# Performance work log

Hardware: AMD Instinct MI355X
Metric: run time of the kernel (lower is better)

## Reference

```python
import jax, jax.numpy as jnp
import numpy as np

H = 64  # hidden size

def _gru_layer(x_tbi, w_ih, w_hh, b_ih, b_hh):
    # x_tbi: [T,B,I]; w_ih: [3H,I]; w_hh: [3H,H]; biases: [3H]
    # Precompute all input projections in one big GEMM: [T,B,3H]
    gx_all = jnp.einsum('tbi,gi->tbg', x_tbi, w_ih) + b_ih

    def step(h, gx):
        gh = h @ w_hh.T + b_hh                      # [B,3H]
        xr, xz, xn = jnp.split(gx, 3, axis=-1)
        hr, hz, hn = jnp.split(gh, 3, axis=-1)
        r = jax.nn.sigmoid(xr + hr)
        z = jax.nn.sigmoid(xz + hz)
        n = jnp.tanh(xn + r * hn)
        h_new = (1.0 - z) * n + z * h
        return h_new, h_new

    B = x_tbi.shape[1]
    h0 = jnp.zeros((B, H), dtype=x_tbi.dtype)
    h_last, out = jax.lax.scan(step, h0, gx_all)     # out: [T,B,H]
    return out, h_last


def setup_inputs() -> dict:
    key = jax.random.key(0)
    ks = jax.random.split(key, 11)
    B, T, I = 2048, 1024, 1
    s0 = 1.0 / np.sqrt(H)  # PyTorch GRU init scale
    u = lambda k, shape: jax.random.uniform(k, shape, jnp.float32, -s0, s0)
    return {
        'x': jax.random.normal(ks[0], (B, T, I), jnp.float32),
        'w_ih0': u(ks[1], (3 * H, I)),
        'w_hh0': u(ks[2], (3 * H, H)),
        'b_ih0': u(ks[3], (3 * H,)),
        'b_hh0': u(ks[4], (3 * H,)),
        'w_ih1': u(ks[5], (3 * H, H)),
        'w_hh1': u(ks[6], (3 * H, H)),
        'b_ih1': u(ks[7], (3 * H,)),
        'b_hh1': u(ks[8], (3 * H,)),
        'w_fc': u(ks[9], (1, H)),
        'b_fc': u(ks[10], (1,)),
    }


def reference(x, w_ih0, w_hh0, b_ih0, b_hh0, w_ih1, w_hh1, b_ih1, b_hh1, w_fc, b_fc):
    # x: [B,T,1] (batch_first) -> scan over time axis
    x_tbi = jnp.transpose(x, (1, 0, 2))              # [T,B,1]
    out0, _ = _gru_layer(x_tbi, w_ih0, w_hh0, b_ih0, b_hh0)   # [T,B,H]
    _, h_last = _gru_layer(out0, w_ih1, w_hh1, b_ih1, b_hh1)  # [B,H]
    # fc(out[:, -1, :]) == fc(h_last of top layer)
    return h_last @ w_fc.T + b_fc                    # [B,1]
```

## Files before the change

kernel.cpp:

```cpp
#include <hip/hip_runtime.h>

#define H    64
#define TT   1024
#define MB   8
#define NW   512
#define NWG  256
#define GSP  584
#define HRUS 144

typedef float  f32x4  __attribute__((ext_vector_type(4)));
typedef __bf16 bf16x8 __attribute__((ext_vector_type(8)));

__device__ __forceinline__ unsigned short bf16_rne(float f) {
    unsigned u = __float_as_uint(f);
    u += 0x7FFFu + ((u >> 16) & 1u);
    return (unsigned short)(u >> 16);
}
__device__ __forceinline__ float fast_sigmoid(float x) {
    return __builtin_amdgcn_rcpf(1.0f + __expf(-x));
}
__device__ __forceinline__ float fast_tanh(float x) {
    float xx = fminf(fmaxf(x, -15.0f), 15.0f);
    float e  = __expf(2.0f * xx);
    return (e - 1.0f) * __builtin_amdgcn_rcpf(e + 1.0f);
}

__global__ __launch_bounds__(NW, 2) void gru_mfma3(
    const float* __restrict__ x,
    const float* __restrict__ w_ih0, const float* __restrict__ w_hh0,
    const float* __restrict__ b_ih0, const float* __restrict__ b_hh0,
    const float* __restrict__ w_ih1, const float* __restrict__ w_hh1,
    const float* __restrict__ b_ih1, const float* __restrict__ b_hh1,
    const float* __restrict__ w_fc,  const float* __restrict__ b_fc,
    float* __restrict__ out)
{
    __shared__ __align__(16) float          xs[MB * TT];
    __shared__ __align__(16) float          gA[MB * GSP];
    __shared__ __align__(16) unsigned short hA[16 * HRUS];

    const int tid  = threadIdx.x;
    const int wave = tid >> 6;
    const int lane = tid & 63;
    const int r    = lane & 15;
    const int q    = lane >> 4;
    const int b0g  = blockIdx.x * MB;

    for (int i = tid; i < 16*HRUS; i += NW) hA[i] = 0;
    for (int i = tid; i < MB*GSP;  i += NW) gA[i] = 0.0f;

    {
        const float* xrow = x + (size_t)(b0g + wave) * TT;
        float* xd = xs + wave * TT;
        #pragma unroll
        for (int u = 0; u < 4; ++u) {
            int idx = (u * 64 + lane) * 4;
            *(float4*)(xd + idx) = *(const float4*)(xrow + idx);
        }
    }

    bf16x8 whi[5][2], wlo[5][2];
    int   doff [5];
    bool  wr_ok[5];
    #pragma unroll
    for (int i = 0; i < 5; ++i) {
        const int n = 5 * wave + i;
        const float* W; int gr;
        if      (n < 12) { W = w_hh0; gr = 16 * n; }
        else if (n < 24) { W = w_ih1; gr = 16 * (n - 12); }
        else if (n < 36) { W = w_hh1; gr = 16 * (n - 24); }
        else             { W = w_hh0; gr = 0; }
        #pragma unroll
        for (int c = 0; c < 2; ++c) {
            const float* wp = W + (gr + r) * H + 32 * c + 8 * q;
            float4 p0 = *(const float4*)wp;
            float4 p1 = *(const float4*)(wp + 4);
            float f[8] = {p0.x,p0.y,p0.z,p0.w,p1.x,p1.y,p1.z,p1.w};
            unsigned short uh[8], ul[8];
            #pragma unroll
            for (int j = 0; j < 8; ++j) {
                unsigned short h16 = bf16_rne(f[j]);
                uh[j] = h16;
                ul[j] = bf16_rne(f[j] - __uint_as_float((unsigned)h16 << 16));
            }
            whi[i][c] = *(const bf16x8*)uh;
            wlo[i][c] = *(const bf16x8*)ul;
        }
        doff [i] = (r & 7) * GSP + 16 * n + 4 * q;
        wr_ok[i] = (n < 36) && ((n < 24) == (r < 8));
    }

    const unsigned short* hp0 = hA + r * HRUS + 8 * q;
    const unsigned short* hp1 = hA + r * HRUS + 8 * (4 + q);
    const unsigned short* hp2 = hp0 + 64;
    const unsigned short* hp3 = hp1 + 64;

    unsigned short* p0h = hA + wave * HRUS + lane;
    unsigned short* p0l = p0h + 64;
    unsigned short* p1h = hA + (wave + 8) * HRUS + lane;
    unsigned short* p1l = p1h + 64;

    const float* gp  = gA + wave * GSP;
    const float* xmy = xs + wave * TT;

    const float wi0r = w_ih0[lane], wi0z = w_ih0[64+lane], wi0n = w_ih0[128+lane];
    const float c0r  = b_ih0[lane]     + b_hh0[lane];
    const float c0z  = b_ih0[64+lane]  + b_hh0[64+lane];
    const float bi0n = b_ih0[128+lane], bh0n = b_hh0[128+lane];
    const float c1r  = b_ih1[lane]     + b_hh1[lane];
    const float c1z  = b_ih1[64+lane]  + b_hh1[64+lane];
    const float bi1n = b_ih1[128+lane], bh1n = b_hh1[128+lane];
    const float wfc  = w_fc[lane];

    float h0reg = 0.0f, h1reg = 0.0f;
    __syncthreads();

    #pragma unroll 1
    for (int t = 0; t < TT; ++t) {
        if (t > 0) {
            float xr = gp[192+lane], xz = gp[256+lane], xn = gp[320+lane];
            float hr = gp[384+lane], hz = gp[448+lane], hn = gp[512+lane];
            float rr = fast_sigmoid(xr + hr + c1r);
            float zz = fast_sigmoid(xz + hz + c1z);
            float nn = fast_tanh(xn + bi1n + rr * (hn + bh1n));
            h1reg = fmaf(zz, h1reg - nn, nn);
            unsigned short hh = bf16_rne(h1reg);
            *p1h = hh;
            *p1l = bf16_rne(h1reg - __uint_as_float((unsigned)hh << 16));
        }
        {
            float xv  = xmy[t];
            float g0r = gp[lane], g0z = gp[64+lane], g0n = gp[128+lane];
            float rr = fast_sigmoid(fmaf(xv, wi0r, c0r) + g0r);
            float zz = fast_sigmoid(fmaf(xv, wi0z, c0z) + g0z);
            float nn = fast_tanh(fmaf(xv, wi0n, bi0n) + rr * (g0n + bh0n));
            h0reg = fmaf(zz, h0reg - nn, nn);
            unsigned short hh = bf16_rne(h0reg);
            *p0h = hh;
            *p0l = bf16_rne(h0reg - __uint_as_float((unsigned)hh << 16));
        }
        __syncthreads();

        {
            bf16x8 hhi0 = *(const bf16x8*)hp0;
            bf16x8 hhi1 = *(const bf16x8*)hp1;
            bf16x8 hlo0 = *(const bf16x8*)hp2;
            bf16x8 hlo1 = *(const bf16x8*)hp3;
            #pragma unroll
            for (int i = 0; i < 5; ++i) {
                f32x4 d = {0.0f, 0.0f, 0.0f, 0.0f};
                d = __builtin_amdgcn_mfma_f32_16x16x32_bf16(whi[i][0], hhi0, d, 0,0,0);
                d = __builtin_amdgcn_mfma_f32_16x16x32_bf16(whi[i][1], hhi1, d, 0,0,0);
                d = __builtin_amdgcn_mfma_f32_16x16x32_bf16(whi[i][0], hlo0, d, 0,0,0);
                d = __builtin_amdgcn_mfma_f32_16x16x32_bf16(whi[i][1], hlo1, d, 0,0,0);
                d = __builtin_amdgcn_mfma_f32_16x16x32_bf16(wlo[i][0], hhi0, d, 0,0,0);
                d = __builtin_amdgcn_mfma_f32_16x16x32_bf16(wlo[i][1], hhi1, d, 0,0,0);
                if (wr_ok[i]) {
                    *(f32x4*)(gA + doff[i]) = d;
                }
            }
        }
        __syncthreads();
    }

    {
        float xr = gp[192+lane], xz = gp[256+lane], xn = gp[320+lane];
        float hr = gp[384+lane], hz = gp[448+lane], hn = gp[512+lane];
        float rr = fast_sigmoid(xr + hr + c1r);
        float zz = fast_sigmoid(xz + hz + c1z);
        float nn = fast_tanh(xn + bi1n + rr * (hn + bh1n));
        h1reg = fmaf(zz, h1reg - nn, nn);
    }
    {
        float v = h1reg * wfc;
        #pragma unroll
        for (int s = 32; s > 0; s >>= 1) v += __shfl_xor(v, s, 64);
        if (lane == 0) out[b0g + wave] = v + b_fc[0];
    }
}

extern "C" void kernel_launch(void* const* d_in, const int* in_sizes, int n_in,
                              void* d_out, int out_size, void* d_ws, size_t ws_size,
                              hipStream_t stream) {
    (void)in_sizes; (void)n_in; (void)out_size; (void)d_ws; (void)ws_size;
    gru_mfma3<<<NWG, NW, 0, stream>>>(
        (const float*)d_in[0],
        (const float*)d_in[1], (const float*)d_in[2],
        (const float*)d_in[3], (const float*)d_in[4],
        (const float*)d_in[5], (const float*)d_in[6],
        (const float*)d_in[7], (const float*)d_in[8],
        (const float*)d_in[9], (const float*)d_in[10],
        (float*)d_out);
}
```

Before: 976.4 us.

## Fuse gate nonlinearity into MFMA waves with double-buffered hidden state, one barrier per step

Waves are split into two groups. Four waves own layer 0 and four own layer 1, and each wave computes a 16-unit slice of all three gates with MFMA and applies the GRU nonlinearity directly from the accumulator registers. This removes the shared-memory gate scratch buffer and its round trip. The hidden state is double-buffered, so each timestep needs one barrier instead of two. The cost is that half of each MFMA tile (rows for batches 8-15) is wasted, and the layer-1 waves do twice the MFMA work of the layer-0 waves, so the load is unbalanced. The final output is reconstructed from the bf16 hi/lo pair instead of the fp32 register, which slightly changes precision.

```diff
diff --git a/kernel.cpp b/kernel.cpp
--- a/kernel.cpp
+++ b/kernel.cpp
@@ -2,10 +2,8 @@
 
 #define H    64
 #define TT   1024
-#define MB   8
 #define NW   512
 #define NWG  256
-#define GSP  584
 #define HRUS 144
 
 typedef float  f32x4  __attribute__((ext_vector_type(4)));
@@ -25,7 +23,7 @@
     return (e - 1.0f) * __builtin_amdgcn_rcpf(e + 1.0f);
 }
 
-__global__ __launch_bounds__(NW, 2) void gru_mfma3(
+__global__ __launch_bounds__(NW, 2) void gru_fuse6(
     const float* __restrict__ x,
     const float* __restrict__ w_ih0, const float* __restrict__ w_hh0,
     const float* __restrict__ b_ih0, const float* __restrict__ b_hh0,
@@ -34,20 +32,24 @@
     const float* __restrict__ w_fc,  const float* __restrict__ b_fc,
     float* __restrict__ out)
 {
-    __shared__ __align__(16) float          xs[MB * TT];
-    __shared__ __align__(16) float          gA[MB * GSP];
-    __shared__ __align__(16) unsigned short hA[16 * HRUS];
+    __shared__ __align__(16) float          xs[8 * TT];
+    __shared__ __align__(16) unsigned short hB[2][16 * HRUS];
 
     const int tid  = threadIdx.x;
     const int wave = tid >> 6;
     const int lane = tid & 63;
     const int r    = lane & 15;
     const int q    = lane >> 4;
-    const int b0g  = blockIdx.x * MB;
-
-    for (int i = tid; i < 16*HRUS; i += NW) hA[i] = 0;
-    for (int i = tid; i < MB*GSP;  i += NW) gA[i] = 0.0f;
-
+    const int b    = r & 7;
+    const int b0g  = blockIdx.x * 8;
+    const bool grpB = (wave >= 4);
+    const int  w4   = wave & 3;
+    const int  jb   = 16 * w4 + 4 * q;
+
+    {
+        unsigned short* hz = &hB[0][0];
+        for (int i = tid; i < 2 * 16 * HRUS; i += NW) hz[i] = 0;
+    }
     {
         const float* xrow = x + (size_t)(b0g + wave) * TT;
         float* xd = xs + wave * TT;
@@ -58,20 +60,14 @@
         }
     }
 
-    bf16x8 whi[5][2], wlo[5][2];
-    int   doff [5];
-    bool  wr_ok[5];
+    bf16x8 whi[6][2], wlo[6][2];
     #pragma unroll
-    for (int i = 0; i < 5; ++i) {
-        const int n = 5 * wave + i;
-        const float* W; int gr;
-        if      (n < 12) { W = w_hh0; gr = 16 * n; }
-        else if (n < 24) { W = w_ih1; gr = 16 * (n - 12); }
-        else if (n < 36) { W = w_hh1; gr = 16 * (n - 24); }
-        else             { W = w_hh0; gr = 0; }
+    for (int i = 0; i < 6; ++i) {
+        const float* W = grpB ? ((i < 3) ? w_ih1 : w_hh1) : w_hh0;
+        const int row0 = 64 * (i % 3) + 16 * w4;
         #pragma unroll
         for (int c = 0; c < 2; ++c) {
-            const float* wp = W + (gr + r) * H + 32 * c + 8 * q;
+            const float* wp = W + (row0 + r) * H + 32 * c + 8 * q;
             float4 p0 = *(const float4*)wp;
             float4 p1 = *(const float4*)(wp + 4);
             float f[8] = {p0.x,p0.y,p0.z,p0.w,p1.x,p1.y,p1.z,p1.w};
@@ -85,93 +81,131 @@
             whi[i][c] = *(const bf16x8*)uh;
             wlo[i][c] = *(const bf16x8*)ul;
         }
-        doff [i] = (r & 7) * GSP + 16 * n + 4 * q;
-        wr_ok[i] = (n < 36) && ((n < 24) == (r < 8));
-    }
-
-    const unsigned short* hp0 = hA + r * HRUS + 8 * q;
-    const unsigned short* hp1 = hA + r * HRUS + 8 * (4 + q);
-    const unsigned short* hp2 = hp0 + 64;
-    const unsigned short* hp3 = hp1 + 64;
-
-    unsigned short* p0h = hA + wave * HRUS + lane;
-    unsigned short* p0l = p0h + 64;
-    unsigned short* p1h = hA + (wave + 8) * HRUS + lane;
-    unsigned short* p1l = p1h + 64;
-
-    const float* gp  = gA + wave * GSP;
-    const float* xmy = xs + wave * TT;
-
-    const float wi0r = w_ih0[lane], wi0z = w_ih0[64+lane], wi0n = w_ih0[128+lane];
-    const float c0r  = b_ih0[lane]     + b_hh0[lane];
-    const float c0z  = b_ih0[64+lane]  + b_hh0[64+lane];
-    const float bi0n = b_ih0[128+lane], bh0n = b_hh0[128+lane];
-    const float c1r  = b_ih1[lane]     + b_hh1[lane];
-    const float c1z  = b_ih1[64+lane]  + b_hh1[64+lane];
-    const float bi1n = b_ih1[128+lane], bh1n = b_hh1[128+lane];
-    const float wfc  = w_fc[lane];
-
-    float h0reg = 0.0f, h1reg = 0.0f;
+    }
+
+    float gwr[4], gwz[4], gwn[4], gcr[4], gcz[4], gbn[4], ghn[4];
+    #pragma unroll
+    for (int k = 0; k < 4; ++k) {
+        const int j = jb + k;
+        if (grpB) {
+            gwr[k] = gwz[k] = gwn[k] = 0.0f;
+            gcr[k] = b_ih1[j]      + b_hh1[j];
+            gcz[k] = b_ih1[64+j]   + b_hh1[64+j];
+            gbn[k] = b_ih1[128+j];
+            ghn[k] = b_hh1[128+j];
+        } else {
+            gwr[k] = w_ih0[j]; gwz[k] = w_ih0[64+j]; gwn[k] = w_ih0[128+j];
+            gcr[k] = b_ih0[j]      + b_hh0[j];
+            gcz[k] = b_ih0[64+j]   + b_hh0[64+j];
+            gbn[k] = b_ih0[128+j];
+            ghn[k] = b_hh0[128+j];
+        }
+    }
+    const float wfc = w_fc[lane];
+
+    float hst[4] = {0.0f, 0.0f, 0.0f, 0.0f};
     __syncthreads();
 
     #pragma unroll 1
-    for (int t = 0; t < TT; ++t) {
-        if (t > 0) {
-            float xr = gp[192+lane], xz = gp[256+lane], xn = gp[320+lane];
-            float hr = gp[384+lane], hz = gp[448+lane], hn = gp[512+lane];
-            float rr = fast_sigmoid(xr + hr + c1r);
-            float zz = fast_sigmoid(xz + hz + c1z);
-            float nn = fast_tanh(xn + bi1n + rr * (hn + bh1n));
-            h1reg = fmaf(zz, h1reg - nn, nn);
-            unsigned short hh = bf16_rne(h1reg);
-            *p1h = hh;
-            *p1l = bf16_rne(h1reg - __uint_as_float((unsigned)hh << 16));
-        }
-        {
-            float xv  = xmy[t];
-            float g0r = gp[lane], g0z = gp[64+lane], g0n = gp[128+lane];
-            float rr = fast_sigmoid(fmaf(xv, wi0r, c0r) + g0r);
-            float zz = fast_sigmoid(fmaf(xv, wi0z, c0z) + g0z);
-            float nn = fast_tanh(fmaf(xv, wi0n, bi0n) + rr * (g0n + bh0n));
-            h0reg = fmaf(zz, h0reg - nn, nn);
-            unsigned short hh = bf16_rne(h0reg);
-            *p0h = hh;
-            *p0l = bf16_rne(h0reg - __uint_as_float((unsigned)hh << 16));
-        }
-        __syncthreads();
-
-        {
-            bf16x8 hhi0 = *(const bf16x8*)hp0;
-            bf16x8 hhi1 = *(const bf16x8*)hp1;
-            bf16x8 hlo0 = *(const bf16x8*)hp2;
-            bf16x8 hlo1 = *(const bf16x8*)hp3;
-            #pragma unroll
-            for (int i = 0; i < 5; ++i) {
-                f32x4 d = {0.0f, 0.0f, 0.0f, 0.0f};
-                d = __builtin_amdgcn_mfma_f32_16x16x32_bf16(whi[i][0], hhi0, d, 0,0,0);
-                d = __builtin_amdgcn_mfma_f32_16x16x32_bf16(whi[i][1], hhi1, d, 0,0,0);
-                d = __builtin_amdgcn_mfma_f32_16x16x32_bf16(whi[i][0], hlo0, d, 0,0,0);
-                d = __builtin_amdgcn_mfma_f32_16x16x32_bf16(whi[i][1], hlo1, d, 0,0,0);
-                d = __builtin_amdgcn_mfma_f32_16x16x32_bf16(wlo[i][0], hhi0, d, 0,0,0);
-                d = __builtin_amdgcn_mfma_f32_16x16x32_bf16(wlo[i][1], hhi1, d, 0,0,0);
-                if (wr_ok[i]) {
-                    *(f32x4*)(gA + doff[i]) = d;
+    for (int t = 0; t <= TT; ++t) {
+        const unsigned short* src = hB[t & 1];
+        unsigned short*       dst = hB[(t + 1) & 1];
+        const bool act = grpB ? (t >= 1) : (t < TT);
+        if (act) {
+            const unsigned short* f0 = src + b * HRUS;
+            const bf16x8 a_h0 = *(const bf16x8*)(f0 + 8 * q);
+            const bf16x8 a_h1 = *(const bf16x8*)(f0 + 32 + 8 * q);
+            const bf16x8 a_l0 = *(const bf16x8*)(f0 + 64 + 8 * q);
+            const bf16x8 a_l1 = *(const bf16x8*)(f0 + 96 + 8 * q);
+
+            f32x4 d0 = {0,0,0,0}, d1 = {0,0,0,0}, d2 = {0,0,0,0};
+            d0 = __builtin_amdgcn_mfma_f32_16x16x32_bf16(whi[0][0], a_h0, d0, 0,0,0);
+            d0 = __builtin_amdgcn_mfma_f32_16x16x32_bf16(whi[0][1], a_h1, d0, 0,0,0);
+            d0 = __builtin_amdgcn_mfma_f32_16x16x32_bf16(whi[0][0], a_l0, d0, 0,0,0);
+            d0 = __builtin_amdgcn_mfma_f32_16x16x32_bf16(whi[0][1], a_l1, d0, 0,0,0);
+            d0 = __builtin_amdgcn_mfma_f32_16x16x32_bf16(wlo[0][0], a_h0, d0, 0,0,0);
+            d0 = __builtin_amdgcn_mfma_f32_16x16x32_bf16(wlo[0][1], a_h1, d0, 0,0,0);
+            d1 = __builtin_amdgcn_mfma_f32_16x16x32_bf16(whi[1][0], a_h0, d1, 0,0,0);
+            d1 = __builtin_amdgcn_mfma_f32_16x16x32_bf16(whi[1][1], a_h1, d1, 0,0,0);
+            d1 = __builtin_amdgcn_mfma_f32_16x16x32_bf16(whi[1][0], a_l0, d1, 0,0,0);
+            d1 = __builtin_amdgcn_mfma_f32_16x16x32_bf16(whi[1][1], a_l1, d1, 0,0,0);
+            d1 = __builtin_amdgcn_mfma_f32_16x16x32_bf16(wlo[1][0], a_h0, d1, 0,0,0);
+            d1 = __builtin_amdgcn_mfma_f32_16x16x32_bf16(wlo[1][1], a_h1, d1, 0,0,0);
+            d2 = __builtin_amdgcn_mfma_f32_16x16x32_bf16(whi[2][0], a_h0, d2, 0,0,0);
+            d2 = __builtin_amdgcn_mfma_f32_16x16x32_bf16(whi[2][1], a_h1, d2, 0,0,0);
+            d2 = __builtin_amdgcn_mfma_f32_16x16x32_bf16(whi[2][0], a_l0, d2, 0,0,0);
+            d2 = __builtin_amdgcn_mfma_f32_16x16x32_bf16(whi[2][1], a_l1, d2, 0,0,0);
+            d2 = __builtin_amdgcn_mfma_f32_16x16x32_bf16(wlo[2][0], a_h0, d2, 0,0,0);
+            d2 = __builtin_amdgcn_mfma_f32_16x16x32_bf16(wlo[2][1], a_h1, d2, 0,0,0);
+
+            if (grpB) {
+                const unsigned short* f1 = src + (8 + b) * HRUS;
+                const bf16x8 c_h0 = *(const bf16x8*)(f1 + 8 * q);
+                const bf16x8 c_h1 = *(const bf16x8*)(f1 + 32 + 8 * q);
+                const bf16x8 c_l0 = *(const bf16x8*)(f1 + 64 + 8 * q);
+                const bf16x8 c_l1 = *(const bf16x8*)(f1 + 96 + 8 * q);
+                f32x4 d3 = {0,0,0,0}, d4 = {0,0,0,0}, d5 = {0,0,0,0};
+                d3 = __builtin_amdgcn_mfma_f32_16x16x32_bf16(whi[3][0], c_h0, d3, 0,0,0);
+                d3 = __builtin_amdgcn_mfma_f32_16x16x32_bf16(whi[3][1], c_h1, d3, 0,0,0);
+                d3 = __builtin_amdgcn_mfma_f32_16x16x32_bf16(whi[3][0], c_l0, d3, 0,0,0);
+                d3 = __builtin_amdgcn_mfma_f32_16x16x32_bf16(whi[3][1], c_l1, d3, 0,0,0);
+                d3 = __builtin_amdgcn_mfma_f32_16x16x32_bf16(wlo[3][0], c_h0, d3, 0,0,0);
+                d3 = __builtin_amdgcn_mfma_f32_16x16x32_bf16(wlo[3][1], c_h1, d3, 0,0,0);
+                d4 = __builtin_amdgcn_mfma_f32_16x16x32_bf16(whi[4][0], c_h0, d4, 0,0,0);
+                d4 = __builtin_amdgcn_mfma_f32_16x16x32_bf16(whi[4][1], c_h1, d4, 0,0,0);
+                d4 = __builtin_amdgcn_mfma_f32_16x16x32_bf16(whi[4][0], c_l0, d4, 0,0,0);
+                d4 = __builtin_amdgcn_mfma_f32_16x16x32_bf16(whi[4][1], c_l1, d4, 0,0,0);
+                d4 = __builtin_amdgcn_mfma_f32_16x16x32_bf16(wlo[4][0], c_h0, d4, 0,0,0);
+                d4 = __builtin_amdgcn_mfma_f32_16x16x32_bf16(wlo[4][1], c_h1, d4, 0,0,0);
+                d5 = __builtin_amdgcn_mfma_f32_16x16x32_bf16(whi[5][0], c_h0, d5, 0,0,0);
+                d5 = __builtin_amdgcn_mfma_f32_16x16x32_bf16(whi[5][1], c_h1, d5, 0,0,0);
+                d5 = __builtin_amdgcn_mfma_f32_16x16x32_bf16(whi[5][0], c_l0, d5, 0,0,0);
+                d5 = __builtin_amdgcn_mfma_f32_16x16x32_bf16(whi[5][1], c_l1, d5, 0,0,0);
+                d5 = __builtin_amdgcn_mfma_f32_16x16x32_bf16(wlo[5][0], c_h0, d5, 0,0,0);
+                d5 = __builtin_amdgcn_mfma_f32_16x16x32_bf16(wlo[5][1], c_h1, d5, 0,0,0);
+                #pragma unroll
+                for (int k = 0; k < 4; ++k) {
+                    float rr = fast_sigmoid(d0[k] + d3[k] + gcr[k]);
+                    float zz = fast_sigmoid(d1[k] + d4[k] + gcz[k]);
+                    float nn = fast_tanh(d2[k] + gbn[k] + rr * (d5[k] + ghn[k]));
+                    hst[k] = fmaf(zz, hst[k] - nn, nn);
+                }
+            } else {
+                const float xv = xs[b * TT + t];
+                #pragma unroll
+                for (int k = 0; k < 4; ++k) {
+                    float rr = fast_sigmoid(fmaf(xv, gwr[k], gcr[k]) + d0[k]);
+                    float zz = fast_sigmoid(fmaf(xv, gwz[k], gcz[k]) + d1[k]);
+                    float nn = fast_tanh(fmaf(xv, gwn[k], gbn[k]) + rr * (d2[k] + ghn[k]));
+                    hst[k] = fmaf(zz, hst[k] - nn, nn);
                 }
             }
+            if (r < 8) {
+                ushort4 hv, lv;
+                {
+                    unsigned short h0_ = bf16_rne(hst[0]);
+                    unsigned short h1_ = bf16_rne(hst[1]);
+                    unsigned short h2_ = bf16_rne(hst[2]);
+                    unsigned short h3_ = bf16_rne(hst[3]);
+                    hv.x = h0_; hv.y = h1_; hv.z = h2_; hv.w = h3_;
+                    lv.x = bf16_rne(hst[0] - __uint_as_float((unsigned)h0_ << 16));
+                    lv.y = bf16_rne(hst[1] - __uint_as_float((unsigned)h1_ << 16));
+                    lv.z = bf16_rne(hst[2] - __uint_as_float((unsigned)h2_ << 16));
+                    lv.w = bf16_rne(hst[3] - __uint_as_float((unsigned)h3_ << 16));
+                }
+                unsigned short* wdst = dst + ((grpB ? 8 : 0) + b) * HRUS + jb;
+                *(ushort4*)(wdst)      = hv;
+                *(ushort4*)(wdst + 64) = lv;
+            }
         }
         __syncthreads();
     }
 
     {
-        float xr = gp[192+lane], xz = gp[256+lane], xn = gp[320+lane];
-        float hr = gp[384+lane], hz = gp[448+lane], hn = gp[512+lane];
-        float rr = fast_sigmoid(xr + hr + c1r);
-        float zz = fast_sigmoid(xz + hz + c1z);
-        float nn = fast_tanh(xn + bi1n + rr * (hn + bh1n));
-        h1reg = fmaf(zz, h1reg - nn, nn);
-    }
-    {
-        float v = h1reg * wfc;
+        const unsigned short* hrow = hB[(TT + 1) & 1] + (8 + wave) * HRUS;
+        float hi = __uint_as_float((unsigned)hrow[lane]      << 16);
+        float lo = __uint_as_float((unsigned)hrow[64 + lane] << 16);
+        float v = (hi + lo) * wfc;
         #pragma unroll
         for (int s = 32; s > 0; s >>= 1) v += __shfl_xor(v, s, 64);
         if (lane == 0) out[b0g + wave] = v + b_fc[0];
@@ -182,7 +216,7 @@
                               void* d_out, int out_size, void* d_ws, size_t ws_size,
                               hipStream_t stream) {
     (void)in_sizes; (void)n_in; (void)out_size; (void)d_ws; (void)ws_size;
-    gru_mfma3<<<NWG, NW, 0, stream>>>(
+    gru_fuse6<<<NWG, NW, 0, stream>>>(
         (const float*)d_in[0],
         (const float*)d_in[1], (const float*)d_in[2],
         (const float*)d_in[3], (const float*)d_in[4],
```

Measured after the change: 1.776 ms. 1.82x slower.
